# Optimization experiments

Hardware: AMD Instinct MI355X
Metric: run time of the kernel (lower is better)

## Reference

```python
import jax, jax.numpy as jnp
import numpy as np

V, D, H, KVH, HD, I, L, T_MAX, THETA = 32000, 1024, 16, 4, 64, 2816, 2, 2048, 10000.0
EPS = 1e-5


def rmsnorm(x, w):
    return x * jax.lax.rsqrt(jnp.mean(x * x, axis=-1, keepdims=True) + EPS) * w


def rope_cos_sin(T):
    inv = 1.0 / (THETA ** (jnp.arange(0, HD, 2, dtype=jnp.float32) / HD))  # [HD/2]
    ang = jnp.arange(T, dtype=jnp.float32)[:, None] * inv[None, :]         # [T, HD/2]
    return jnp.cos(ang), jnp.sin(ang)


def apply_rope(x, cos, sin):
    # x: [B, T, h, HD]; interleaved complex pairs as in torch.view_as_complex
    x0 = x[..., 0::2]
    x1 = x[..., 1::2]
    c = cos[None, :, None, :]
    s = sin[None, :, None, :]
    o0 = x0 * c - x1 * s
    o1 = x0 * s + x1 * c
    return jnp.stack([o0, o1], axis=-1).reshape(x.shape)


def setup_inputs() -> dict:
    key = jax.random.key(0)
    ks = jax.random.split(key, 12)
    sc = 0.02
    return {
        "toks": jax.random.randint(ks[0], (1, 2048), 0, V),
        "embed": jax.random.normal(ks[1], (V, D), jnp.float32) * sc,
        "Wq": jax.random.normal(ks[2], (L, D, H * HD), jnp.float32) * sc,
        "Wk": jax.random.normal(ks[3], (L, D, KVH * HD), jnp.float32) * sc,
        "Wv": jax.random.normal(ks[4], (L, D, KVH * HD), jnp.float32) * sc,
        "Wo": jax.random.normal(ks[5], (L, H * HD, D), jnp.float32) * sc,
        "Wgate": jax.random.normal(ks[6], (L, D, I), jnp.float32) * sc,
        "Wup": jax.random.normal(ks[7], (L, D, I), jnp.float32) * sc,
        "Wdown": jax.random.normal(ks[8], (L, I, D), jnp.float32) * sc,
        "ln1_w": jnp.ones((L, D), jnp.float32),
        "ln2_w": jnp.ones((L, D), jnp.float32),
        "norm_w": jnp.ones((D,), jnp.float32),
        "Wlm": jax.random.normal(ks[9], (D, V), jnp.float32) * sc,
    }


def reference(toks, embed, Wq, Wk, Wv, Wo, Wgate, Wup, Wdown, ln1_w, ln2_w, norm_w, Wlm):
    B, T = toks.shape
    cos, sin = rope_cos_sin(T)
    causal = jnp.tril(jnp.ones((T, T), dtype=bool))
    add_mask = jnp.where(causal, 0.0, -jnp.inf).astype(jnp.float32)  # [T, T]
    n_rep = H // KVH
    scale = 1.0 / np.sqrt(HD)

    x = embed[toks]  # [B, T, D]
    for l in range(L):
        h = rmsnorm(x, ln1_w[l])
        q = (h @ Wq[l]).reshape(B, T, H, HD)
        k = (h @ Wk[l]).reshape(B, T, KVH, HD)
        v = (h @ Wv[l]).reshape(B, T, KVH, HD)
        q = apply_rope(q, cos, sin)
        k = apply_rope(k, cos, sin)
        k = jnp.repeat(k, n_rep, axis=2)  # GQA repeat_kv -> [B, T, H, HD]
        v = jnp.repeat(v, n_rep, axis=2)
        # materialized scores [B, H, T, T] (faithful to source)
        scores = jnp.einsum('bqhd,bkhd->bhqk', q, k) * scale + add_mask[None, None]
        probs = jax.nn.softmax(scores, axis=-1)
        attn = jnp.einsum('bhqk,bkhd->bqhd', probs, v).reshape(B, T, H * HD)
        x = x + attn @ Wo[l]
        h = rmsnorm(x, ln2_w[l])
        x = x + (jax.nn.silu(h @ Wgate[l]) * (h @ Wup[l])) @ Wdown[l]

    x = rmsnorm(x, norm_w)
    return x @ Wlm  # [B, T, V]
```

## Files before the change

### kernel.cpp

```cpp
#include <hip/hip_runtime.h>

#define T_SEQ 2048
#define DMODEL 1024
#define NH 16
#define NKV 4
#define HEAD_DIM 64
#define FFDIM 2816
#define NVOCAB 32000

#define QBLK 128
#define KBLK 128
#define KSS 72
#define VTS 136
#define PSS 136

using u16 = unsigned short;
typedef __bf16 bf16x8 __attribute__((ext_vector_type(8)));
typedef float f32x4 __attribute__((ext_vector_type(4)));

__device__ __forceinline__ float b2f(u16 u) {
    union { unsigned int i; float f; } v; v.i = ((unsigned int)u) << 16; return v.f;
}
__device__ __forceinline__ u16 f2b(float f) {
    unsigned int u = __builtin_bit_cast(unsigned int, f);
    unsigned int r = (u + 0x7FFFu + ((u >> 16) & 1u)) >> 16;
    return (u16)r;
}
__device__ __forceinline__ void gload16(const u16* g, u16* l) {
    __builtin_amdgcn_global_load_lds(
        (const __attribute__((address_space(1))) void*)g,
        (__attribute__((address_space(3))) void*)l, 16, 0, 0);
}

__global__ __launch_bounds__(256) void embed_rms_kernel(const int* __restrict__ toks,
                                                        const float* __restrict__ emb,
                                                        const float* __restrict__ w,
                                                        float* __restrict__ x,
                                                        u16* __restrict__ h) {
    __shared__ float red[256];
    const int row = blockIdx.x, tid = threadIdx.x;
    const float* er = emb + (size_t)toks[row] * DMODEL;
    float vals[4]; float ss = 0.f;
#pragma unroll
    for (int i = 0; i < 4; i++) {
        float v = er[tid + 256 * i];
        vals[i] = v; ss += v * v;
        x[(size_t)row * DMODEL + tid + 256 * i] = v;
    }
    red[tid] = ss; __syncthreads();
    for (int s = 128; s > 0; s >>= 1) { if (tid < s) red[tid] += red[tid + s]; __syncthreads(); }
    float inv = rsqrtf(red[0] * (1.0f / DMODEL) + 1e-5f);
#pragma unroll
    for (int i = 0; i < 4; i++) {
        int c = tid + 256 * i;
        h[(size_t)row * DMODEL + c] = f2b(vals[i] * inv * w[c]);
    }
}

__global__ __launch_bounds__(256) void rmsnorm_kernel(const float* __restrict__ x,
                                                      const float* __restrict__ w,
                                                      u16* __restrict__ out) {
    __shared__ float red[256];
    const int row = blockIdx.x, tid = threadIdx.x;
    const float* xr = x + (size_t)row * DMODEL;
    float vals[4]; float ss = 0.f;
#pragma unroll
    for (int i = 0; i < 4; i++) { float v = xr[tid + 256 * i]; vals[i] = v; ss += v * v; }
    red[tid] = ss; __syncthreads();
    for (int s = 128; s > 0; s >>= 1) { if (tid < s) red[tid] += red[tid + s]; __syncthreads(); }
    float inv = rsqrtf(red[0] * (1.0f / DMODEL) + 1e-5f);
#pragma unroll
    for (int i = 0; i < 4; i++) {
        int c = tid + 256 * i;
        out[(size_t)row * DMODEL + c] = f2b(vals[i] * inv * w[c]);
    }
}

__global__ __launch_bounds__(256) void tcast_kernel(const float* __restrict__ in,
                                                    u16* __restrict__ out, int K, int N,
                                                    size_t in_ls, size_t out_ls) {
    __shared__ float tile[32][33];
    in += (size_t)blockIdx.z * in_ls;
    out += (size_t)blockIdx.z * out_ls;
    int bx = blockIdx.x * 32;
    int by = blockIdx.y * 32;
    int tx = threadIdx.x & 31, ty = threadIdx.x >> 5;
#pragma unroll
    for (int i = 0; i < 32; i += 8)
        tile[ty + i][tx] = in[(size_t)(by + ty + i) * N + bx + tx];
    __syncthreads();
#pragma unroll
    for (int i = 0; i < 32; i += 8)
        out[(size_t)(bx + ty + i) * K + by + tx] = f2b(tile[tx][ty + i]);
}

__global__ __launch_bounds__(256) void tcast_gu_kernel(const float* __restrict__ Wg,
                                                       const float* __restrict__ Wu,
                                                       u16* __restrict__ out,
                                                       size_t w_ls, size_t out_ls) {
    __shared__ float tg[32][17], tu[32][17];
    Wg += (size_t)blockIdx.z * w_ls;
    Wu += (size_t)blockIdx.z * w_ls;
    out += (size_t)blockIdx.z * out_ls;
    const int Q = blockIdx.x;
    const int KY = blockIdx.y * 32;
    const int tid = threadIdx.x;
    const int tx = tid & 15, ty = tid >> 4;
#pragma unroll
    for (int i = 0; i < 32; i += 16) {
        tg[ty + i][tx] = Wg[(size_t)(KY + ty + i) * FFDIM + Q * 16 + tx];
        tu[ty + i][tx] = Wu[(size_t)(KY + ty + i) * FFDIM + Q * 16 + tx];
    }
    __syncthreads();
    const int tx2 = tid & 31, ty2 = tid >> 5;
#pragma unroll
    for (int i = 0; i < 32; i += 8) {
        int r = ty2 + i;
        float v = (r < 16) ? tg[tx2][r] : tu[tx2][r - 16];
        out[(size_t)(Q * 32 + r) * DMODEL + KY + tx2] = f2b(v);
    }
}

__global__ __launch_bounds__(256) void rope_table_kernel(float2* __restrict__ tbl) {
    int idx = blockIdx.x * 256 + threadIdx.x;
    int t = idx >> 5, i = idx & 31;
    float inv = expf(-(float)i * (9.210340371976184f / 32.0f));
    float ang = (float)t * inv;
    tbl[idx] = make_float2(cosf(ang), sinf(ang));
}

__global__ __launch_bounds__(256) void ropeall_kernel(const u16* __restrict__ fqkv,
                                                      const float2* __restrict__ tbl,
                                                      u16* __restrict__ qb,
                                                      u16* __restrict__ kb,
                                                      u16* __restrict__ vt) {
    __shared__ u16 tile[32][33];
    const int bid = blockIdx.x, tid = threadIdx.x;
    if (bid < 5120) {
        int i, t, hh, coloff;
        u16* out;
        size_t rest;
        if (bid < 4096) {
            int idx = bid * 256 + tid;
            i = idx & 31; rest = idx >> 5;
            t = (int)(rest >> 4); hh = (int)(rest & 15); coloff = 0; out = qb;
        } else {
            int idx = (bid - 4096) * 256 + tid;
            i = idx & 31; rest = idx >> 5;
            t = (int)(rest >> 2); hh = (int)(rest & 3); coloff = 1024; out = kb;
        }
        float2 cs = tbl[t * 32 + i];
        size_t src = (size_t)t * 1536 + coloff + hh * HEAD_DIM + 2 * i;
        size_t dst = rest * HEAD_DIM + 2 * i;
        float x0 = b2f(fqkv[src]), x1 = b2f(fqkv[src + 1]);
        out[dst]     = f2b(x0 * cs.x - x1 * cs.y);
        out[dst + 1] = f2b(x0 * cs.y + x1 * cs.x);
    } else {
        int b2 = bid - 5120;
        int bx = (b2 & 7) * 32;
        int by = (b2 >> 3) * 32;
        int tx = tid & 31, ty = tid >> 5;
#pragma unroll
        for (int i = 0; i < 32; i += 8)
            tile[ty + i][tx] = fqkv[(size_t)(by + ty + i) * 1536 + 1280 + bx + tx];
        __syncthreads();
#pragma unroll
        for (int i = 0; i < 32; i += 8)
            vt[(size_t)(bx + ty + i) * T_SEQ + by + tx] = tile[tx][ty + i];
    }
}

template<bool OUT_BF16, bool ADD>
__global__ __launch_bounds__(256) void gemm_bt_kernel(const u16* __restrict__ A,
                                                      const u16* __restrict__ BT,
                                                      void* __restrict__ Cp,
                                                      int N, int K) {
    __shared__ __align__(16) u16 As[2][128 * 32];
    __shared__ __align__(16) u16 Bs[2][128 * 32];
    const int tid = threadIdx.x;
    const int gx = gridDim.x;
    const int nwg = gx * gridDim.y;
    const int hwid = blockIdx.y * gx + blockIdx.x;
    const int q = nwg >> 3, r = nwg & 7;
    const int xcd = hwid & 7, rem = hwid >> 3;
    const int wgid = (xcd < r ? xcd * (q + 1) : r * (q + 1) + (xcd - r) * q) + rem;
    const int brow = wgid % gx, bcol = wgid / gx;

    const int w = tid >> 6, lane = tid & 63;
    const int wr = w >> 1, wc = w & 1;
    const int lg = lane >> 4, lr = lane & 15;

    f32x4 acc[4][4] = {};

    const int srow = w * 32 + (lane >> 2);
    const int scol = (lane & 3) << 3;
    const u16* gA = A + (size_t)(brow * 128 + srow) * K + scol;
    const u16* gB = BT + (size_t)(bcol * 128 + srow) * K + scol;
    const size_t koff16 = (size_t)16 * K;
    const int lofs0 = (w * 32) * 32;
    const int lofs1 = (w * 32 + 16) * 32;

    const int nt = K >> 5;
    gload16(gA, &As[0][lofs0]);
    gload16(gA + koff16, &As[0][lofs1]);
    gload16(gB, &Bs[0][lofs0]);
    gload16(gB + koff16, &Bs[0][lofs1]);
    __syncthreads();

    int cur = 0;
    for (int t = 0; t < nt; t++) {
        if (t + 1 < nt) {
            const int kb = (t + 1) << 5;
            gload16(gA + kb, &As[cur ^ 1][lofs0]);
            gload16(gA + koff16 + kb, &As[cur ^ 1][lofs1]);
            gload16(gB + kb, &Bs[cur ^ 1][lofs0]);
            gload16(gB + koff16 + kb, &Bs[cur ^ 1][lofs1]);
        }
        bf16x8 aF[4], bF[4];
#pragma unroll
        for (int m = 0; m < 4; m++)
            aF[m] = *(const bf16x8*)(&As[cur][(wr * 64 + m * 16 + lr) * 32 + lg * 8]);
#pragma unroll
        for (int n = 0; n < 4; n++)
            bF[n] = *(const bf16x8*)(&Bs[cur][(wc * 64 + n * 16 + lr) * 32 + lg * 8]);
#pragma unroll
        for (int m = 0; m < 4; m++)
#pragma unroll
            for (int n = 0; n < 4; n++)
                acc[m][n] = __builtin_amdgcn_mfma_f32_16x16x32_bf16(aF[m], bF[n], acc[m][n], 0, 0, 0);
        __syncthreads();
        cur ^= 1;
    }

#pragma unroll
    for (int m = 0; m < 4; m++)
#pragma unroll
        for (int n = 0; n < 4; n++)
#pragma unroll
            for (int j = 0; j < 4; j++) {
                int row = brow * 128 + wr * 64 + m * 16 + lg * 4 + j;
                int col = bcol * 128 + wc * 64 + n * 16 + lr;
                size_t idx = (size_t)row * N + col;
                float v = acc[m][n][j];
                if constexpr (OUT_BF16) {
                    ((u16*)Cp)[idx] = f2b(v);
                } else if constexpr (ADD) {
                    ((float*)Cp)[idx] = ((const float*)Cp)[idx] + v;
                } else {
                    ((float*)Cp)[idx] = v;
                }
            }
}

template<int MODE>
__global__ __launch_bounds__(512) void gemm256_kernel(const u16* __restrict__ A,
                                                      const u16* __restrict__ BT,
                                                      void* __restrict__ Cp,
                                                      int Nout, int K) {
    extern __shared__ __align__(16) u16 lds[];
    const int tid = threadIdx.x;
    const int gx = gridDim.x;
    const int nwg = gx * gridDim.y;
    const int hwid = blockIdx.y * gx + blockIdx.x;
    const int q = nwg >> 3, r = nwg & 7;
    const int xcd = hwid & 7, rem = hwid >> 3;
    const int wgid = (xcd < r ? xcd * (q + 1) : r * (q + 1) + (xcd - r) * q) + rem;
    const int bR = wgid % gx, bC = wgid / gx;

    const int w = tid >> 6, lane = tid & 63;
    const int wm = w >> 2, wn = w & 3;
    const int lg = lane >> 4, lr = lane & 15;

    f32x4 acc[8][4] = {};

    const int srow = lane >> 2;
    const int scol = ((lane & 3) ^ ((lane >= 32) ? 2 : 0)) << 3;
    const int rblk = (((lr >= 8) ? (lg ^ 2) : lg)) << 4;

    const u16* Ab = A + (size_t)(bR * 256) * K + scol;
    const u16* Bb = BT + (size_t)(bC * 256) * K + scol;

    auto STAGE_A = [&](int t, int b) {
        gload16(Ab + (size_t)(w * 16 + srow) * K + t * 32,
                lds + (b * 16384 + w * 1024) / 2);
        gload16(Ab + (size_t)((w + 8) * 16 + srow) * K + t * 32,
                lds + (b * 16384 + (w + 8) * 1024) / 2);
    };
    auto STAGE_B = [&](int t, int b) {
        gload16(Bb + (size_t)(w * 16 + srow) * K + t * 32,
                lds + (32768 + b * 16384 + w * 1024) / 2);
        gload16(Bb + (size_t)((w + 8) * 16 + srow) * K + t * 32,
                lds + (32768 + b * 16384 + (w + 8) * 1024) / 2);
    };

    const int nt = K >> 5;
    STAGE_A(0, 0); STAGE_B(0, 0);
    asm volatile("s_waitcnt vmcnt(0)" ::: "memory");
    __builtin_amdgcn_s_barrier();

    int cur = 0;
    for (int t = 0; t < nt; t++) {
        const bool st = (t + 1 < nt);
        const int nb = cur ^ 1;
        bf16x8 bF[4];
        {
            bf16x8 aF[4];
#pragma unroll
            for (int mi = 0; mi < 4; mi++)
                aF[mi] = *(const bf16x8*)((const char*)lds + cur * 16384 +
                                          (wm * 8 + mi) * 1024 + lr * 64 + rblk);
#pragma unroll
            for (int n = 0; n < 4; n++)
                bF[n] = *(const bf16x8*)((const char*)lds + 32768 + cur * 16384 +
                                         (wn * 4 + n) * 1024 + lr * 64 + rblk);
            if (st) STAGE_A(t + 1, nb);
            __builtin_amdgcn_s_barrier();
            asm volatile("s_waitcnt lgkmcnt(0)" ::: "memory");
            __builtin_amdgcn_sched_barrier(0);
            __builtin_amdgcn_s_setprio(1);
#pragma unroll
            for (int mi = 0; mi < 4; mi++)
#pragma unroll
                for (int n = 0; n < 4; n++)
                    acc[mi][n] = __builtin_amdgcn_mfma_f32_16x16x32_bf16(
                        aF[mi], bF[n], acc[mi][n], 0, 0, 0);
            __builtin_amdgcn_s_setprio(0);
            __builtin_amdgcn_s_barrier();
        }
        {
            bf16x8 aF[4];
#pragma unroll
            for (int mi = 0; mi < 4; mi++)
                aF[mi] = *(const bf16x8*)((const char*)lds + cur * 16384 +
                                          (wm * 8 + 4 + mi) * 1024 + lr * 64 + rblk);
            if (st) STAGE_B(t + 1, nb);
            asm volatile("s_waitcnt vmcnt(0)" ::: "memory");
            __builtin_amdgcn_s_barrier();
            asm volatile("s_waitcnt lgkmcnt(0)" ::: "memory");
            __builtin_amdgcn_sched_barrier(0);
            __builtin_amdgcn_s_setprio(1);
#pragma unroll
            for (int mi = 0; mi < 4; mi++)
#pragma unroll
                for (int n = 0; n < 4; n++)
                    acc[4 + mi][n] = __builtin_amdgcn_mfma_f32_16x16x32_bf16(
                        aF[mi], bF[n], acc[4 + mi][n], 0, 0, 0);
            __builtin_amdgcn_s_setprio(0);
            __builtin_amdgcn_s_barrier();
        }
        cur ^= 1;
    }

#pragma unroll
    for (int m = 0; m < 8; m++) {
        if constexpr (MODE == 0) {
#pragma unroll
            for (int n = 0; n < 4; n++)
#pragma unroll
                for (int jj = 0; jj < 4; jj++) {
                    int row = bR * 256 + wm * 128 + m * 16 + lg * 4 + jj;
                    int col = bC * 256 + wn * 64 + n * 16 + lr;
                    ((float*)Cp)[(size_t)row * Nout + col] = acc[m][n][jj];
                }
        } else {
#pragma unroll
            for (int n = 0; n < 4; n += 2)
#pragma unroll
                for (int jj = 0; jj < 4; jj++) {
                    int row = bR * 256 + wm * 128 + m * 16 + lg * 4 + jj;
                    int col = bC * 128 + wn * 32 + (n >> 1) * 16 + lr;
                    float g = acc[m][n][jj], u = acc[m][n + 1][jj];
                    float s = g / (1.f + __expf(-g));
                    ((u16*)Cp)[(size_t)row * Nout + col] = f2b(s * u);
                }
        }
    }
}

__device__ __forceinline__ int bs_off(int c, int k) {
    return c * 40 + ((((k >> 3) ^ ((c >> 3) & 3)) << 3) | (k & 7));
}

__global__ __launch_bounds__(256) void gemm_f32b_kernel(const u16* __restrict__ A,
                                                        const float* __restrict__ B,
                                                        float* __restrict__ C,
                                                        int N, int K) {
    __shared__ __align__(16) u16 As[128 * 40];
    __shared__ __align__(16) u16 Bs[128 * 40];
    const int tid = threadIdx.x;
    const int brow = blockIdx.y, bcol = blockIdx.x;
    const int wid = tid >> 6, lane = tid & 63;
    const int wr = wid >> 1, wc = wid & 1;
    const int lg = lane >> 4, lr = lane & 15;

    f32x4 acc[4][4] = {};
    const int ar = tid >> 2, ac = (tid & 3) << 3;
    const int bk = tid >> 4, bc = (tid & 15) << 3;

    for (int kb = 0; kb < K; kb += 32) {
        {
            const u16* ga = A + (size_t)(brow * 128 + ar) * K + kb + ac;
            *(uint4*)(&As[ar * 40 + ac]) = *(const uint4*)ga;
            *(uint4*)(&As[(ar + 64) * 40 + ac]) = *(const uint4*)(ga + (size_t)64 * K);
        }
        {
            const float* gb = B + (size_t)(kb + bk) * N + bcol * 128 + bc;
            float4 a0 = *(const float4*)gb;
            float4 a1 = *(const float4*)(gb + 4);
            float4 b0 = *(const float4*)(gb + (size_t)16 * N);
            float4 b1 = *(const float4*)(gb + (size_t)16 * N + 4);
            float f0[8] = {a0.x, a0.y, a0.z, a0.w, a1.x, a1.y, a1.z, a1.w};
            float f1[8] = {b0.x, b0.y, b0.z, b0.w, b1.x, b1.y, b1.z, b1.w};
#pragma unroll
            for (int i = 0; i < 8; i++) {
                Bs[bs_off(bc + i, bk)] = f2b(f0[i]);
                Bs[bs_off(bc + i, bk + 16)] = f2b(f1[i]);
            }
        }
        __syncthreads();

        bf16x8 aF[4], bF[4];
#pragma unroll
        for (int m = 0; m < 4; m++)
            aF[m] = *(const bf16x8*)(&As[(wr * 64 + m * 16 + lr) * 40 + lg * 8]);
#pragma unroll
        for (int n = 0; n < 4; n++) {
            int c = wc * 64 + n * 16 + lr;
            bF[n] = *(const bf16x8*)(&Bs[c * 40 + ((lg ^ ((c >> 3) & 3)) << 3)]);
        }
#pragma unroll
        for (int m = 0; m < 4; m++)
#pragma unroll
            for (int n = 0; n < 4; n++)
                acc[m][n] = __builtin_amdgcn_mfma_f32_16x16x32_bf16(aF[m], bF[n], acc[m][n], 0, 0, 0);
        __syncthreads();
    }

#pragma unroll
    for (int m = 0; m < 4; m++)
#pragma unroll
        for (int n = 0; n < 4; n++)
#pragma unroll
            for (int j = 0; j < 4; j++) {
                int row = brow * 128 + wr * 64 + m * 16 + lg * 4 + j;
                int col = bcol * 128 + wc * 64 + n * 16 + lr;
                C[(size_t)row * N + col] = acc[m][n][j];
            }
}

__global__ __launch_bounds__(512) void fattn_kernel(const u16* __restrict__ q,
                                                    const u16* __restrict__ k,
                                                    const u16* __restrict__ vt,
                                                    u16* __restrict__ out) {
    extern __shared__ __align__(16) u16 smem[];
    u16* Ks = smem;
    u16* Vt = smem + KBLK * KSS;
    u16* Ps = Vt + HEAD_DIM * VTS;
    const int tid = threadIdx.x;
    const int qb0 = blockIdx.x * QBLK, h = blockIdx.y, kvh = h >> 2;
    const int w = tid >> 6, lane = tid & 63;
    const int lg = lane >> 4, lr = lane & 15;

    bf16x8 qf0, qf1;
    {
        const u16* src = q + ((size_t)(qb0 + w * 16 + lr) * NH + h) * HEAD_DIM;
        qf0 = *(const bf16x8*)(src + lg * 8);
        qf1 = *(const bf16x8*)(src + 32 + lg * 8);
    }

    f32x4 acc_o[4] = {};
    float m_run[4] = {-1e30f, -1e30f, -1e30f, -1e30f};
    float l_run[4] = {0.f, 0.f, 0.f, 0.f};

    const int ntiles = blockIdx.x + 1;

    for (int kt = 0; kt < ntiles; kt++) {
        const int kb = kt * KBLK;
        __syncthreads();
        for (int c = tid; c < KBLK * 8; c += 512) {
            int row = c >> 3, c8 = (c & 7) << 3;
            *(uint4*)(&Ks[row * KSS + c8]) =
                *(const uint4*)(k + ((size_t)(kb + row) * NKV + kvh) * HEAD_DIM + c8);
        }
        for (int c = tid; c < HEAD_DIM * 16; c += 512) {
            int d = c >> 4, c16 = (c & 15) << 3;
            *(uint4*)(&Vt[d * VTS + c16]) =
                *(const uint4*)(vt + (size_t)(kvh * HEAD_DIM + d) * T_SEQ + kb + c16);
        }
        __syncthreads();

        f32x4 s[8] = {};
#pragma unroll
        for (int n = 0; n < 8; n++) {
            bf16x8 kf0 = *(const bf16x8*)(&Ks[(n * 16 + lr) * KSS + lg * 8]);
            bf16x8 kf1 = *(const bf16x8*)(&Ks[(n * 16 + lr) * KSS + 32 + lg * 8]);
            s[n] = __builtin_amdgcn_mfma_f32_16x16x32_bf16(qf0, kf0, s[n], 0, 0, 0);
            s[n] = __builtin_amdgcn_mfma_f32_16x16x32_bf16(qf1, kf1, s[n], 0, 0, 0);
        }

#pragma unroll
        for (int j = 0; j < 4; j++) {
            int q_g = qb0 + w * 16 + lg * 4 + j;
            float sv[8];
            float tmax = -1e30f;
#pragma unroll
            for (int n = 0; n < 8; n++) {
                float xx = s[n][j] * 0.125f;
                if (kb + n * 16 + lr > q_g) xx = -1e30f;
                sv[n] = xx;
                tmax = fmaxf(tmax, xx);
            }
#pragma unroll
            for (int mm = 1; mm < 16; mm <<= 1) tmax = fmaxf(tmax, __shfl_xor(tmax, mm));
            float mn = fmaxf(m_run[j], tmax);
            float sc = __expf(m_run[j] - mn);
            m_run[j] = mn;
            float rsum = 0.f;
#pragma unroll
            for (int n = 0; n < 8; n++) {
                float p = __expf(sv[n] - mn);
                rsum += p;
                Ps[(w * 16 + lg * 4 + j) * PSS + n * 16 + lr] = f2b(p);
            }
#pragma unroll
            for (int mm = 1; mm < 16; mm <<= 1) rsum += __shfl_xor(rsum, mm);
            l_run[j] = l_run[j] * sc + rsum;
#pragma unroll
            for (int n = 0; n < 4; n++) acc_o[n][j] *= sc;
        }

#pragma unroll
        for (int ks = 0; ks < 4; ks++) {
            bf16x8 pf = *(const bf16x8*)(&Ps[(w * 16 + lr) * PSS + ks * 32 + lg * 8]);
#pragma unroll
            for (int n = 0; n < 4; n++) {
                bf16x8 vf = *(const bf16x8*)(&Vt[(n * 16 + lr) * VTS + ks * 32 + lg * 8]);
                acc_o[n] = __builtin_amdgcn_mfma_f32_16x16x32_bf16(pf, vf, acc_o[n], 0, 0, 0);
            }
        }
    }

#pragma unroll
    for (int n = 0; n < 4; n++)
#pragma unroll
        for (int j = 0; j < 4; j++) {
            int t = qb0 + w * 16 + lg * 4 + j;
            int d = n * 16 + lr;
            out[((size_t)t * NH + h) * HEAD_DIM + d] = f2b(acc_o[n][j] / l_run[j]);
        }
}

extern "C" void kernel_launch(void* const* d_in, const int* in_sizes, int n_in,
                              void* d_out, int out_size, void* d_ws, size_t ws_size,
                              hipStream_t stream) {
    const int*   toks = (const int*)d_in[0];
    const float* emb  = (const float*)d_in[1];
    const float* Wq   = (const float*)d_in[2];
    const float* Wk   = (const float*)d_in[3];
    const float* Wv   = (const float*)d_in[4];
    const float* Wo   = (const float*)d_in[5];
    const float* Wg   = (const float*)d_in[6];
    const float* Wu   = (const float*)d_in[7];
    const float* Wd   = (const float*)d_in[8];
    const float* ln1  = (const float*)d_in[9];
    const float* ln2  = (const float*)d_in[10];
    const float* nw   = (const float*)d_in[11];
    const float* Wlm  = (const float*)d_in[12];

    char* ob = (char*)d_out;
    const size_t MB = 1024 * 1024;
    float* x    = (float*)(ob + 0 * MB);
    u16* fqkv   = (u16*)  (ob + 8 * MB);
    float2* tbl = (float2*)(ob + 16 * MB);
    u16* vt     = (u16*)  (ob + 40 * MB);
    u16* qb     = (u16*)  (ob + 42 * MB);
    u16* kb     = (u16*)  (ob + 47 * MB);
    u16* attnb  = (u16*)  (ob + 48 * MB);
    u16* ffb    = (u16*)  (ob + 52 * MB);
    u16* Wt = (u16*)(ob + 64 * MB);
    const size_t OFF_QKV = 0;
    const size_t OFF_O   = (size_t)1536 * 1024;
    const size_t OFF_GU  = OFF_O + (size_t)1024 * 1024;
    const size_t OFF_D   = OFF_GU + (size_t)5632 * 1024;
    const size_t LS      = OFF_D + (size_t)2816 * 1024;
    u16* h = (u16*)d_ws;
    bool ws_big = ws_size >= 72 * MB;
    u16* WlmT = ws_big ? (u16*)((char*)d_ws + 4 * MB) : nullptr;
    (void)in_sizes; (void)n_in; (void)out_size;

    dim3 blk(256);
    auto tc = [&](const float* in, u16* out, int K, int N, size_t in_ls, int nz) {
        tcast_kernel<<<dim3(N / 32, K / 32, nz), blk, 0, stream>>>(in, out, K, N, in_ls, LS);
    };
    auto gemm_f32 = [&](const u16* A, const u16* BT, float* C, int N, int K, bool add) {
        dim3 g(T_SEQ / 128, N / 128);
        if (add) gemm_bt_kernel<false, true><<<g, blk, 0, stream>>>(A, BT, (void*)C, N, K);
        else     gemm_bt_kernel<false, false><<<g, blk, 0, stream>>>(A, BT, (void*)C, N, K);
    };
    auto gemm_b16 = [&](const u16* A, const u16* BT, u16* C, int N, int K) {
        dim3 g(T_SEQ / 128, N / 128);
        gemm_bt_kernel<true, false><<<g, blk, 0, stream>>>(A, BT, (void*)C, N, K);
    };

    tc(Wq, Wt + OFF_QKV,                       DMODEL, NH * HEAD_DIM,  (size_t)DMODEL * NH * HEAD_DIM, 2);
    tc(Wk, Wt + OFF_QKV + (size_t)1024 * 1024, DMODEL, NKV * HEAD_DIM, (size_t)DMODEL * NKV * HEAD_DIM, 2);
    tc(Wv, Wt + OFF_QKV + (size_t)1280 * 1024, DMODEL, NKV * HEAD_DIM, (size_t)DMODEL * NKV * HEAD_DIM, 2);
    tc(Wo, Wt + OFF_O,                         DMODEL, DMODEL,         (size_t)DMODEL * DMODEL, 2);
    tcast_gu_kernel<<<dim3(FFDIM / 16, DMODEL / 32, 2), blk, 0, stream>>>(
        Wg, Wu, Wt + OFF_GU, (size_t)DMODEL * FFDIM, LS);
    tc(Wd, Wt + OFF_D,                         FFDIM,  DMODEL,         (size_t)FFDIM * DMODEL, 2);
    if (WlmT)
        tcast_kernel<<<dim3(NVOCAB / 32, DMODEL / 32, 1), blk, 0, stream>>>(
            Wlm, WlmT, DMODEL, NVOCAB, 0, 0);
    rope_table_kernel<<<dim3(T_SEQ * 32 / 256), blk, 0, stream>>>(tbl);

    (void)hipFuncSetAttribute(reinterpret_cast<const void*>(gemm256_kernel<0>),
                              hipFuncAttributeMaxDynamicSharedMemorySize, 65536);
    (void)hipFuncSetAttribute(reinterpret_cast<const void*>(gemm256_kernel<3>),
                              hipFuncAttributeMaxDynamicSharedMemorySize, 65536);
    const int FATTN_LDS = (KBLK * KSS + HEAD_DIM * VTS + QBLK * PSS) * 2;
    (void)hipFuncSetAttribute(reinterpret_cast<const void*>(fattn_kernel),
                              hipFuncAttributeMaxDynamicSharedMemorySize, FATTN_LDS);

    embed_rms_kernel<<<dim3(T_SEQ), blk, 0, stream>>>(toks, emb, ln1, x, h);

    for (int l = 0; l < 2; l++) {
        const u16* WqkvT = Wt + (size_t)l * LS + OFF_QKV;
        const u16* WoT   = Wt + (size_t)l * LS + OFF_O;
        const u16* WguT  = Wt + (size_t)l * LS + OFF_GU;
        const u16* WdT   = Wt + (size_t)l * LS + OFF_D;

        if (l > 0)
            rmsnorm_kernel<<<dim3(T_SEQ), blk, 0, stream>>>(x, ln1 + (size_t)l * DMODEL, h);
        gemm_b16(h, WqkvT, fqkv, 1536, DMODEL);
        ropeall_kernel<<<dim3(5632), blk, 0, stream>>>(fqkv, tbl, qb, kb, vt);
        fattn_kernel<<<dim3(T_SEQ / QBLK, NH), dim3(512), FATTN_LDS, stream>>>(qb, kb, vt, attnb);
        gemm_f32(attnb, WoT, x, DMODEL, DMODEL, true);

        rmsnorm_kernel<<<dim3(T_SEQ), blk, 0, stream>>>(x, ln2 + (size_t)l * DMODEL, h);
        {
            dim3 g(T_SEQ / 256, 5632 / 256);
            gemm256_kernel<3><<<g, dim3(512), 65536, stream>>>(h, WguT, (void*)ffb,
                                                               FFDIM, DMODEL);
        }
        gemm_f32(ffb, WdT, x, DMODEL, FFDIM, true);
    }

    rmsnorm_kernel<<<dim3(T_SEQ), blk, 0, stream>>>(x, nw, h);
    if (WlmT) {
        dim3 g(T_SEQ / 256, NVOCAB / 256);
        gemm256_kernel<0><<<g, dim3(512), 65536, stream>>>(h, WlmT, (void*)d_out,
                                                           NVOCAB, DMODEL);
    } else {
        dim3 g(NVOCAB / 128, T_SEQ / 128);
        gemm_f32b_kernel<<<g, blk, 0, stream>>>(h, Wlm, (float*)d_out, NVOCAB, DMODEL);
    }
}
```

Baseline: 825.2 us.

## Shrink gemm256 tile to 128x256 with triple-buffered LDS pipeline

Cuts the M tile of the 256-tile GEMM from 256 to 128 rows, which halves the accumulators per wave. It replaces the double-buffered two-half loop with a three-stage LDS ring that prefetches two K-steps ahead using partial vmcnt waits. Launch bounds now request 4 waves per SIMD, and the grid doubles along M for the FFN gate/up and LM-head GEMMs. Less reuse per block means more global traffic for B, in exchange for higher occupancy, deeper latency hiding and more blocks to fill the CUs.

```diff
diff --git a/kernel.cpp b/kernel.cpp
--- a/kernel.cpp
+++ b/kernel.cpp
@@ -253,10 +253,10 @@
 }
 
 template<int MODE>
-__global__ __launch_bounds__(512) void gemm256_kernel(const u16* __restrict__ A,
-                                                      const u16* __restrict__ BT,
-                                                      void* __restrict__ Cp,
-                                                      int Nout, int K) {
+__global__ __launch_bounds__(512, 4) void gemm256_kernel(const u16* __restrict__ A,
+                                                         const u16* __restrict__ BT,
+                                                         void* __restrict__ Cp,
+                                                         int Nout, int K) {
     extern __shared__ __align__(16) u16 lds[];
     const int tid = threadIdx.x;
     const int gx = gridDim.x;
@@ -271,94 +271,70 @@
     const int wm = w >> 2, wn = w & 3;
     const int lg = lane >> 4, lr = lane & 15;
 
-    f32x4 acc[8][4] = {};
+    f32x4 acc[4][4] = {};
 
     const int srow = lane >> 2;
     const int scol = ((lane & 3) ^ ((lane >= 32) ? 2 : 0)) << 3;
     const int rblk = (((lr >= 8) ? (lg ^ 2) : lg)) << 4;
 
-    const u16* Ab = A + (size_t)(bR * 256) * K + scol;
+    const u16* Ab = A + (size_t)(bR * 128) * K + scol;
     const u16* Bb = BT + (size_t)(bC * 256) * K + scol;
 
-    auto STAGE_A = [&](int t, int b) {
+    auto STAGE = [&](int t, int b) {
         gload16(Ab + (size_t)(w * 16 + srow) * K + t * 32,
-                lds + (b * 16384 + w * 1024) / 2);
-        gload16(Ab + (size_t)((w + 8) * 16 + srow) * K + t * 32,
-                lds + (b * 16384 + (w + 8) * 1024) / 2);
+                lds + (b * 8192 + w * 1024) / 2);
+        gload16(Bb + (size_t)(w * 16 + srow) * K + t * 32,
+                lds + (24576 + b * 16384 + w * 1024) / 2);
+        gload16(Bb + (size_t)((w + 8) * 16 + srow) * K + t * 32,
+                lds + (24576 + b * 16384 + (w + 8) * 1024) / 2);
     };
-    auto STAGE_B = [&](int t, int b) {
-        gload16(Bb + (size_t)(w * 16 + srow) * K + t * 32,
-                lds + (32768 + b * 16384 + w * 1024) / 2);
-        gload16(Bb + (size_t)((w + 8) * 16 + srow) * K + t * 32,
-                lds + (32768 + b * 16384 + (w + 8) * 1024) / 2);
-    };
 
     const int nt = K >> 5;
-    STAGE_A(0, 0); STAGE_B(0, 0);
-    asm volatile("s_waitcnt vmcnt(0)" ::: "memory");
+    STAGE(0, 0); STAGE(1, 1);
+    asm volatile("s_waitcnt vmcnt(3)" ::: "memory");
     __builtin_amdgcn_s_barrier();
 
     int cur = 0;
     for (int t = 0; t < nt; t++) {
-        const bool st = (t + 1 < nt);
-        const int nb = cur ^ 1;
-        bf16x8 bF[4];
-        {
-            bf16x8 aF[4];
-#pragma unroll
-            for (int mi = 0; mi < 4; mi++)
-                aF[mi] = *(const bf16x8*)((const char*)lds + cur * 16384 +
-                                          (wm * 8 + mi) * 1024 + lr * 64 + rblk);
+        const bool st = (t + 2 < nt);
+        const int nb = (cur >= 1) ? cur - 1 : cur + 2;
+        bf16x8 aF[4], bF[4];
+#pragma unroll
+        for (int mi = 0; mi < 4; mi++)
+            aF[mi] = *(const bf16x8*)((const char*)lds + cur * 8192 +
+                                      (wm * 4 + mi) * 1024 + lr * 64 + rblk);
+#pragma unroll
+        for (int n = 0; n < 4; n++)
+            bF[n] = *(const bf16x8*)((const char*)lds + 24576 + cur * 16384 +
+                                     (wn * 4 + n) * 1024 + lr * 64 + rblk);
+        if (st) STAGE(t + 2, nb);
+        if (t + 1 < nt) {
+            if (st) asm volatile("s_waitcnt vmcnt(3)" ::: "memory");
+            else    asm volatile("s_waitcnt vmcnt(0)" ::: "memory");
+        }
+        __builtin_amdgcn_s_barrier();
+        asm volatile("s_waitcnt lgkmcnt(0)" ::: "memory");
+        __builtin_amdgcn_sched_barrier(0);
+        __builtin_amdgcn_s_setprio(1);
+#pragma unroll
+        for (int mi = 0; mi < 4; mi++)
 #pragma unroll
             for (int n = 0; n < 4; n++)
-                bF[n] = *(const bf16x8*)((const char*)lds + 32768 + cur * 16384 +
-                                         (wn * 4 + n) * 1024 + lr * 64 + rblk);
-            if (st) STAGE_A(t + 1, nb);
-            __builtin_amdgcn_s_barrier();
-            asm volatile("s_waitcnt lgkmcnt(0)" ::: "memory");
-            __builtin_amdgcn_sched_barrier(0);
-            __builtin_amdgcn_s_setprio(1);
-#pragma unroll
-            for (int mi = 0; mi < 4; mi++)
-#pragma unroll
-                for (int n = 0; n < 4; n++)
-                    acc[mi][n] = __builtin_amdgcn_mfma_f32_16x16x32_bf16(
-                        aF[mi], bF[n], acc[mi][n], 0, 0, 0);
-            __builtin_amdgcn_s_setprio(0);
-            __builtin_amdgcn_s_barrier();
-        }
-        {
-            bf16x8 aF[4];
-#pragma unroll
-            for (int mi = 0; mi < 4; mi++)
-                aF[mi] = *(const bf16x8*)((const char*)lds + cur * 16384 +
-                                          (wm * 8 + 4 + mi) * 1024 + lr * 64 + rblk);
-            if (st) STAGE_B(t + 1, nb);
-            asm volatile("s_waitcnt vmcnt(0)" ::: "memory");
-            __builtin_amdgcn_s_barrier();
-            asm volatile("s_waitcnt lgkmcnt(0)" ::: "memory");
-            __builtin_amdgcn_sched_barrier(0);
-            __builtin_amdgcn_s_setprio(1);
-#pragma unroll
-            for (int mi = 0; mi < 4; mi++)
-#pragma unroll
-                for (int n = 0; n < 4; n++)
-                    acc[4 + mi][n] = __builtin_amdgcn_mfma_f32_16x16x32_bf16(
-                        aF[mi], bF[n], acc[4 + mi][n], 0, 0, 0);
-            __builtin_amdgcn_s_setprio(0);
-            __builtin_amdgcn_s_barrier();
-        }
-        cur ^= 1;
-    }
-
-#pragma unroll
-    for (int m = 0; m < 8; m++) {
+                acc[mi][n] = __builtin_amdgcn_mfma_f32_16x16x32_bf16(
+                    aF[mi], bF[n], acc[mi][n], 0, 0, 0);
+        __builtin_amdgcn_s_setprio(0);
+        __builtin_amdgcn_s_barrier();
+        cur = (cur == 2) ? 0 : cur + 1;
+    }
+
+#pragma unroll
+    for (int m = 0; m < 4; m++) {
         if constexpr (MODE == 0) {
 #pragma unroll
             for (int n = 0; n < 4; n++)
 #pragma unroll
                 for (int jj = 0; jj < 4; jj++) {
-                    int row = bR * 256 + wm * 128 + m * 16 + lg * 4 + jj;
+                    int row = bR * 128 + wm * 64 + m * 16 + lg * 4 + jj;
                     int col = bC * 256 + wn * 64 + n * 16 + lr;
                     ((float*)Cp)[(size_t)row * Nout + col] = acc[m][n][jj];
                 }
@@ -367,7 +343,7 @@
             for (int n = 0; n < 4; n += 2)
 #pragma unroll
                 for (int jj = 0; jj < 4; jj++) {
-                    int row = bR * 256 + wm * 128 + m * 16 + lg * 4 + jj;
+                    int row = bR * 128 + wm * 64 + m * 16 + lg * 4 + jj;
                     int col = bC * 128 + wn * 32 + (n >> 1) * 16 + lr;
                     float g = acc[m][n][jj], u = acc[m][n + 1][jj];
                     float s = g / (1.f + __expf(-g));
@@ -615,9 +591,9 @@
     rope_table_kernel<<<dim3(T_SEQ * 32 / 256), blk, 0, stream>>>(tbl);
 
     (void)hipFuncSetAttribute(reinterpret_cast<const void*>(gemm256_kernel<0>),
-                              hipFuncAttributeMaxDynamicSharedMemorySize, 65536);
+                              hipFuncAttributeMaxDynamicSharedMemorySize, 73728);
     (void)hipFuncSetAttribute(reinterpret_cast<const void*>(gemm256_kernel<3>),
-                              hipFuncAttributeMaxDynamicSharedMemorySize, 65536);
+                              hipFuncAttributeMaxDynamicSharedMemorySize, 73728);
     const int FATTN_LDS = (KBLK * KSS + HEAD_DIM * VTS + QBLK * PSS) * 2;
     (void)hipFuncSetAttribute(reinterpret_cast<const void*>(fattn_kernel),
                               hipFuncAttributeMaxDynamicSharedMemorySize, FATTN_LDS);
@@ -639,8 +615,8 @@
 
         rmsnorm_kernel<<<dim3(T_SEQ), blk, 0, stream>>>(x, ln2 + (size_t)l * DMODEL, h);
         {
-            dim3 g(T_SEQ / 256, 5632 / 256);
-            gemm256_kernel<3><<<g, dim3(512), 65536, stream>>>(h, WguT, (void*)ffb,
+            dim3 g(T_SEQ / 128, 5632 / 256);
+            gemm256_kernel<3><<<g, dim3(512), 73728, stream>>>(h, WguT, (void*)ffb,
                                                                FFDIM, DMODEL);
         }
         gemm_f32(ffb, WdT, x, DMODEL, FFDIM, true);
@@ -648,8 +624,8 @@
 
     rmsnorm_kernel<<<dim3(T_SEQ), blk, 0, stream>>>(x, nw, h);
     if (WlmT) {
-        dim3 g(T_SEQ / 256, NVOCAB / 256);
-        gemm256_kernel<0><<<g, dim3(512), 65536, stream>>>(h, WlmT, (void*)d_out,
+        dim3 g(T_SEQ / 128, NVOCAB / 256);
+        gemm256_kernel<0><<<g, dim3(512), 73728, stream>>>(h, WlmT, (void*)d_out,
                                                            NVOCAB, DMODEL);
     } else {
         dim3 g(NVOCAB / 128, T_SEQ / 128);
```

New measurement: 768.8 us. 6.8% less time.
